# Optimization experiments

Hardware: AMD Instinct MI355X
Metric: run time of the kernel (lower is better)

Reference implementation:

```python
import jax, jax.numpy as jnp
import numpy as np

H = 128  # hidden_dim


def _lstm_dir(x, w_ih, w_hh, b, reverse):
    """Single-direction LSTM over x:[B,T,I]. PyTorch gate order (i,f,g,o)."""
    B = x.shape[0]
    gx = jnp.einsum('bti,gi->btg', x, w_ih) + b        # [B,T,4H] input-side gates, one batched GEMM
    gx = jnp.swapaxes(gx, 0, 1)                        # [T,B,4H]
    if reverse:
        gx = gx[::-1]

    def step(carry, g_x):
        h, c = carry
        g = g_x + h @ w_hh.T                           # [B,4H]
        i, f, gg, o = jnp.split(g, 4, axis=-1)
        i = jax.nn.sigmoid(i)
        f = jax.nn.sigmoid(f)
        gg = jnp.tanh(gg)
        o = jax.nn.sigmoid(o)
        c = f * c + i * gg
        h = o * jnp.tanh(c)
        return (h, c), h

    init = (jnp.zeros((B, H), x.dtype), jnp.zeros((B, H), x.dtype))
    (hT, cT), hs = jax.lax.scan(step, init, gx)        # hs:[T,B,H]
    hs = jnp.swapaxes(hs, 0, 1)                        # [B,T,H]
    if reverse:
        hs = hs[:, ::-1]
    return hs, hT, cT


def _bilstm_layer(x, pf, pb):
    hf, hTf, cTf = _lstm_dir(x, *pf, reverse=False)
    hb, hTb, cTb = _lstm_dir(x, *pb, reverse=True)
    return jnp.concatenate([hf, hb], axis=-1), (hTf, cTf), (hTb, cTb)


def setup_inputs() -> dict:
    key = jax.random.key(0)
    ks = jax.random.split(key, 13)
    s = 1.0 / np.sqrt(H)
    B, T, I = 256, 512, 24
    d = {"x": jax.random.normal(ks[0], (B, T, I), jnp.float32)}
    # layer 0 input dim = 24; layer 1 input dim = 2*H = 256
    dims = {"l0f": I, "l0b": I, "l1f": 2 * H, "l1b": 2 * H}
    i = 1
    for tag, din in dims.items():
        d[f"w_ih_{tag}"] = jax.random.uniform(ks[i], (4 * H, din), jnp.float32, -s, s); i += 1
        d[f"w_hh_{tag}"] = jax.random.uniform(ks[i], (4 * H, H), jnp.float32, -s, s); i += 1
        d[f"b_{tag}"] = jax.random.uniform(ks[i], (4 * H,), jnp.float32, -s, s); i += 1
    return d


def reference(x,
              w_ih_l0f, w_hh_l0f, b_l0f, w_ih_l0b, w_hh_l0b, b_l0b,
              w_ih_l1f, w_hh_l1f, b_l1f, w_ih_l1b, w_hh_l1b, b_l1b):
    # Layer 0 (bidirectional)
    y0, (hTf0, cTf0), (hTb0, cTb0) = _bilstm_layer(
        x, (w_ih_l0f, w_hh_l0f, b_l0f), (w_ih_l0b, w_hh_l0b, b_l0b))
    # Inter-layer dropout is identity in eval mode.
    # Layer 1 (bidirectional)
    y1, (hTf1, cTf1), (hTb1, cTb1) = _bilstm_layer(
        y0, (w_ih_l1f, w_hh_l1f, b_l1f), (w_ih_l1b, w_hh_l1b, b_l1b))
    # PyTorch h_n/c_n layout: [num_layers*num_dirs, B, H] ordered l0f,l0b,l1f,l1b
    h_n = jnp.stack([hTf0, hTb0, hTf1, hTb1], axis=0)
    c_n = jnp.stack([cTf0, cTb0, cTf1, cTb1], axis=0)
    return y1, h_n, c_n
```

## Files before the change

### kernel.cpp

```cpp
#include <hip/hip_runtime.h>
#include <hip/hip_bf16.h>
#include <stdint.h>

#define Bn 256
#define Tn 512
#define Hn 128
#define G4 512
#define Mn (Bn*Tn)

typedef __attribute__((ext_vector_type(8))) short s16x8;
typedef __attribute__((ext_vector_type(4))) float f32x4;

__device__ __forceinline__ float b2f(unsigned short u) {
    union { unsigned int i; float f; } v; v.i = ((unsigned int)u) << 16; return v.f;
}
__device__ __forceinline__ unsigned short f2b(float f) {
    union { float f; unsigned int i; } v; v.f = f;
    unsigned int x = v.i;
    unsigned int r = (x + 0x7FFFu + ((x >> 16) & 1u)) >> 16;
    return (unsigned short)r;
}
__device__ __forceinline__ unsigned int pk2(float a, float b) {
    __hip_bfloat162 t = __float22bfloat162_rn(make_float2(a, b));
    union { __hip_bfloat162 v; unsigned int u; } c; c.v = t; return c.u;
}
__device__ __forceinline__ s16x8 cvt8v(const float* p) {
    f32x4 a = *(const f32x4*)p;
    f32x4 b = *(const f32x4*)(p + 4);
    s16x8 r;
    r[0] = (short)f2b(a[0]); r[1] = (short)f2b(a[1]);
    r[2] = (short)f2b(a[2]); r[3] = (short)f2b(a[3]);
    r[4] = (short)f2b(b[0]); r[5] = (short)f2b(b[1]);
    r[6] = (short)f2b(b[2]); r[7] = (short)f2b(b[3]);
    return r;
}
__device__ __forceinline__ float sigm(float x) {
    return __builtin_amdgcn_rcpf(1.f + __expf(-x));
}
__device__ __forceinline__ float tanh_f(float x) {
    return 1.f - 2.f * __builtin_amdgcn_rcpf(1.f + __expf(2.f * x));
}
__device__ __forceinline__ void gload16(const void* gsrc, void* lds) {
    __builtin_amdgcn_global_load_lds(
        (const __attribute__((address_space(1))) unsigned int*)gsrc,
        (__attribute__((address_space(3))) unsigned int*)lds, 16, 0, 0);
}
__device__ __forceinline__ void ldsbar() {
    asm volatile("s_waitcnt lgkmcnt(0)\n\ts_barrier" ::: "memory");
}

__global__ __launch_bounds__(256)
void prep(const float* __restrict__ x,
          const float* __restrict__ w0f, const float* __restrict__ w0b,
          const float* __restrict__ w1f, const float* __restrict__ w1b,
          unsigned short* __restrict__ xb,
          unsigned short* __restrict__ w0bf,
          unsigned short* __restrict__ w1bf)
{
    int tid = blockIdx.x * 256 + threadIdx.x;
    int nthr = gridDim.x * 256;
    for (int idx = tid; idx < Mn * 32; idx += nthr) {
        int row = idx >> 5, col = idx & 31;
        xb[idx] = f2b(col < 24 ? x[row * 24 + col] : 0.f);
    }
    for (int idx = tid; idx < 2 * 512 * 32; idx += nthr) {
        int d = idx >> 14, rem = idx & 16383;
        int n = rem >> 5, col = rem & 31;
        const float* w = d ? w0b : w0f;
        w0bf[idx] = f2b(col < 24 ? w[n * 24 + col] : 0.f);
    }
    for (int idx = tid; idx < 2 * 512 * 256; idx += nthr) {
        int d = idx >> 17, rem = idx & 131071;
        const float* w = d ? w1b : w1f;
        w1bf[idx] = f2b(w[rem]);
    }
}

template<int BK, int KOUT>
__global__ __launch_bounds__(256, 2)
void gemm_tile(const unsigned short* __restrict__ A, int lda,
               const unsigned short* __restrict__ W,
               unsigned short* __restrict__ gx)
{
    constexpr int GR = BK / 8;
    constexpr int SWM = (GR >= 8) ? 7 : (GR - 1);
    constexpr int ASZ = 128 * BK * 2;
    constexpr int GOFF = (BK == 128) ? 0 : 2 * ASZ;
    constexpr int SMEM = 2 * ASZ + ((BK == 128) ? 0 : 4 * 16 * 68 * 4);
    __shared__ char smem[SMEM];
    unsigned short* Atile = (unsigned short*)smem;
    unsigned short* Btile = (unsigned short*)(smem + ASZ);

    const int K = BK * KOUT;
    const int mb = blockIdx.x;
    const int nb = blockIdx.y;
    const int dir = nb >> 2, ncol0 = (nb & 3) * 128;
    const int row0 = mb * 128;
    const unsigned short* Asrc = A + (size_t)row0 * lda;
    const unsigned short* Bsrc = W + (size_t)dir * 512 * K + (size_t)ncol0 * K;
    unsigned short* out = gx + (size_t)dir * Mn * G4;

    const int tid = threadIdx.x;
    const int w = tid >> 6, l = tid & 63;
    const int q = l >> 4, i = l & 15;
    const int wm = w >> 1, wn = w & 1;

    f32x4 acc[4][4];
#pragma unroll
    for (int a = 0; a < 4; ++a)
#pragma unroll
        for (int b = 0; b < 4; ++b) acc[a][b] = f32x4{0.f, 0.f, 0.f, 0.f};

    for (int ko = 0; ko < KOUT; ++ko) {
#pragma unroll
        for (int it = 0; it < (128 * GR) / 256; ++it) {
            int g = it * 256 + tid;
            int row = g / GR, p = g % GR;
            int gi = p ^ (row & SWM);
            gload16(Asrc + (size_t)row * lda + ko * BK + gi * 8,
                    (char*)Atile + g * 16);
        }
#pragma unroll
        for (int it = 0; it < (128 * GR) / 256; ++it) {
            int g = it * 256 + tid;
            int row = g / GR, p = g % GR;
            int gi = p ^ (row & SWM);
            gload16(Bsrc + (size_t)row * K + ko * BK + gi * 8,
                    (char*)Btile + g * 16);
        }
        __syncthreads();
#pragma unroll
        for (int kf = 0; kf < BK / 32; ++kf) {
            s16x8 af[4], bf[4];
#pragma unroll
            for (int mt = 0; mt < 4; ++mt) {
                int ar = wm * 64 + mt * 16 + i;
                int p = (kf * 4 + q) ^ (ar & SWM);
                af[mt] = *(const s16x8*)((char*)Atile + (ar * GR + p) * 16);
            }
#pragma unroll
            for (int nt = 0; nt < 4; ++nt) {
                int br = wn * 64 + nt * 16 + i;
                int p = (kf * 4 + q) ^ (br & SWM);
                bf[nt] = *(const s16x8*)((char*)Btile + (br * GR + p) * 16);
            }
#pragma unroll
            for (int mt = 0; mt < 4; ++mt)
#pragma unroll
                for (int nt = 0; nt < 4; ++nt)
                    acc[mt][nt] = __builtin_amdgcn_mfma_f32_16x16x32_bf16(
                        af[mt], bf[nt], acc[mt][nt], 0, 0, 0);
        }
        __syncthreads();
    }

    float* gbufw = (float*)(smem + GOFF) + w * (16 * 68);
#pragma unroll
    for (int mt = 0; mt < 4; ++mt) {
#pragma unroll
        for (int nt = 0; nt < 4; ++nt)
#pragma unroll
            for (int r = 0; r < 4; ++r)
                gbufw[(q * 4 + r) * 68 + nt * 16 + i] = acc[mt][nt][r];
        __syncthreads();
#pragma unroll
        for (int it2 = 0; it2 < 2; ++it2) {
            int rr = (l >> 3) + it2 * 8;
            int cc = (l & 7) * 8;
            const float* gsrc = gbufw + rr * 68 + cc;
            uint4 pv;
            pv.x = pk2(gsrc[0], gsrc[1]);
            pv.y = pk2(gsrc[2], gsrc[3]);
            pv.z = pk2(gsrc[4], gsrc[5]);
            pv.w = pk2(gsrc[6], gsrc[7]);
            *(uint4*)(out + (size_t)(row0 + wm * 64 + mt * 16 + rr) * G4
                          + ncol0 + wn * 64 + cc) = pv;
        }
        __syncthreads();
    }
}

template<int LAYER>
__global__ __launch_bounds__(256, 1)
void lstm_rec(const unsigned short* __restrict__ gx,
              const float* __restrict__ Whf,
              const float* __restrict__ Whb,
              const float* __restrict__ biasf,
              const float* __restrict__ biasb,
              float* __restrict__ y,
              unsigned short* __restrict__ y0b,
              float* __restrict__ hn,
              float* __restrict__ cn)
{
    const int b0  = blockIdx.x * 2;
    const int dir = blockIdx.y;
    const float* Wh   = dir ? Whb : Whf;
    const float* bias = dir ? biasb : biasf;
    const unsigned short* gxd = gx + (size_t)dir * Mn * G4;

    const int tid = threadIdx.x;
    const int w = tid >> 6;
    const int l = tid & 63;
    const int q = l >> 4, i = l & 15;
    const int u = q & 1;
    const int r = q >> 1;
    const int j = 32 * w + 16 * u + i;
    const int b = b0 + r;

    __shared__ __align__(16) unsigned short hbuf[2][160];

    for (int idx = tid; idx < 2 * 160; idx += 256)
        ((unsigned short*)hbuf)[idx] = 0;

    s16x8 wh[4][2][4];
#pragma unroll
    for (int g = 0; g < 4; ++g)
#pragma unroll
        for (int ut = 0; ut < 2; ++ut) {
            int n = 128 * g + 32 * w + 16 * ut + i;
#pragma unroll
            for (int kf = 0; kf < 4; ++kf)
                wh[g][ut][kf] = cvt8v(Wh + (size_t)n * Hn + kf * 32 + q * 8);
        }

    const float bi = bias[j],       bfv = bias[128 + j];
    const float bg = bias[256 + j], bo  = bias[384 + j];
    float c = 0.f, hlast = 0.f;

    const s16x8* ah0p = (const s16x8*)&hbuf[i >> 3][0 * 32 + q * 8];
    const s16x8* ah1p = (const s16x8*)&hbuf[i >> 3][1 * 32 + q * 8];
    const s16x8* ah2p = (const s16x8*)&hbuf[i >> 3][2 * 32 + q * 8];
    const s16x8* ah3p = (const s16x8*)&hbuf[i >> 3][3 * 32 + q * 8];
    unsigned short* hw = &hbuf[r][j];

    const intptr_t gstep = dir ? -(intptr_t)G4 : (intptr_t)G4;
    const unsigned short* p0 =
        gxd + ((size_t)b * Tn + (dir ? Tn - 1 : 0)) * G4 + j;
    const unsigned short* gp_pre = p0 + 8 * gstep;
    const intptr_t ystep = dir ? (intptr_t)-256 : (intptr_t)256;
    float* yp = y + ((size_t)b * Tn + (dir ? Tn - 1 : 0)) * 256 + dir * 128 + j;
    unsigned short* y0p =
        y0b + ((size_t)b * Tn + (dir ? Tn - 1 : 0)) * 256 + dir * 128 + j;

    unsigned short bufA[4][8], bufB[4][8];
#pragma unroll
    for (int f = 0; f < 8; ++f) {
        const unsigned short* gp = p0 + f * gstep;
        bufA[0][f] = gp[0];
        bufA[1][f] = gp[128];
        bufA[2][f] = gp[256];
        bufA[3][f] = gp[384];
    }

    __syncthreads();

    auto do8 = [&](unsigned short (&useB)[4][8], unsigned short (&ldB)[4][8],
                   int sb) {
#pragma unroll
        for (int f = 0; f < 8; ++f) {
            const int s = sb + f;

            s16x8 ah0 = *ah0p, ah1 = *ah1p, ah2 = *ah2p, ah3 = *ah3p;

            ldB[0][f] = gp_pre[0];
            ldB[1][f] = gp_pre[128];
            ldB[2][f] = gp_pre[256];
            ldB[3][f] = gp_pre[384];
            if (s < Tn - 9) gp_pre += gstep;
            const float pi = b2f(useB[0][f]) + bi;
            const float pf = b2f(useB[1][f]) + bfv;
            const float pg = b2f(useB[2][f]) + bg;
            const float po = b2f(useB[3][f]) + bo;

            f32x4 acc[4][2];
#pragma unroll
            for (int g = 0; g < 4; ++g)
#pragma unroll
                for (int ut = 0; ut < 2; ++ut)
                    acc[g][ut] = f32x4{0.f, 0.f, 0.f, 0.f};
#pragma unroll
            for (int g = 0; g < 4; ++g)
#pragma unroll
                for (int ut = 0; ut < 2; ++ut)
                    acc[g][ut] = __builtin_amdgcn_mfma_f32_16x16x32_bf16(
                        ah0, wh[g][ut][0], acc[g][ut], 0, 0, 0);
#pragma unroll
            for (int g = 0; g < 4; ++g)
#pragma unroll
                for (int ut = 0; ut < 2; ++ut)
                    acc[g][ut] = __builtin_amdgcn_mfma_f32_16x16x32_bf16(
                        ah1, wh[g][ut][1], acc[g][ut], 0, 0, 0);
#pragma unroll
            for (int g = 0; g < 4; ++g)
#pragma unroll
                for (int ut = 0; ut < 2; ++ut)
                    acc[g][ut] = __builtin_amdgcn_mfma_f32_16x16x32_bf16(
                        ah2, wh[g][ut][2], acc[g][ut], 0, 0, 0);
#pragma unroll
            for (int g = 0; g < 4; ++g)
#pragma unroll
                for (int ut = 0; ut < 2; ++ut)
                    acc[g][ut] = __builtin_amdgcn_mfma_f32_16x16x32_bf16(
                        ah3, wh[g][ut][3], acc[g][ut], 0, 0, 0);

            const float s_i = u ? acc[0][1][0] : acc[0][0][0];
            const float s_f = u ? acc[1][1][0] : acc[1][0][0];
            const float s_g = u ? acc[2][1][0] : acc[2][0][0];
            const float s_o = u ? acc[3][1][0] : acc[3][0][0];

            float g_i = s_i + pi;
            float g_f = s_f + pf;
            float g_g = s_g + pg;
            float g_o = s_o + po;
            float iv = sigm(g_i), fv = sigm(g_f), ov = sigm(g_o);
            float gv = tanh_f(g_g);
            c = fv * c + iv * gv;
            float h = ov * tanh_f(c);
            hlast = h;
            unsigned int hp;
            asm("v_cvt_pk_bf16_f32 %0, %1, %2" : "=v"(hp) : "v"(h), "v"(h));
            unsigned short hb = (unsigned short)hp;
            *hw = hb;
            if (LAYER == 0) *y0p = hb;
            else            *yp  = h;
            yp += ystep; y0p += ystep;

            ldsbar();
        }
    };

    for (int sb = 0; sb < Tn; sb += 16) {
        do8(bufA, bufB, sb);
        do8(bufB, bufA, sb + 8);
    }

    const int slot = LAYER * 2 + dir;
    hn[((size_t)slot * Bn + b) * Hn + j] = hlast;
    cn[((size_t)slot * Bn + b) * Hn + j] = c;
}

extern "C" void kernel_launch(void* const* d_in, const int* in_sizes, int n_in,
                              void* d_out, int out_size, void* d_ws, size_t ws_size,
                              hipStream_t stream)
{
    const float* x     = (const float*)d_in[0];
    const float* wih0f = (const float*)d_in[1];
    const float* whh0f = (const float*)d_in[2];
    const float* b0f   = (const float*)d_in[3];
    const float* wih0b = (const float*)d_in[4];
    const float* whh0b = (const float*)d_in[5];
    const float* b0b   = (const float*)d_in[6];
    const float* wih1f = (const float*)d_in[7];
    const float* whh1f = (const float*)d_in[8];
    const float* b1f   = (const float*)d_in[9];
    const float* wih1b = (const float*)d_in[10];
    const float* whh1b = (const float*)d_in[11];
    const float* b1b   = (const float*)d_in[12];

    float* y  = (float*)d_out;
    float* hn = y + (size_t)Mn * 256;
    float* cn = hn + (size_t)4 * Bn * Hn;
    unsigned short* gx = (unsigned short*)d_ws;

    unsigned short* scr  = (unsigned short*)d_out;
    unsigned short* y0b  = scr;
    unsigned short* xb   = scr + (size_t)Mn * 256;
    unsigned short* w0bf = xb  + (size_t)Mn * 32;
    unsigned short* w1bf = w0bf + 2 * 512 * 32;

    prep<<<2048, 256, 0, stream>>>(x, wih0f, wih0b, wih1f, wih1b, xb, w0bf, w1bf);

    dim3 gg(1024, 8), gb(256);
    dim3 rg(128, 2), rb(256);

    gemm_tile<32, 1><<<gg, gb, 0, stream>>>(xb, 32, w0bf, gx);
    lstm_rec<0><<<rg, rb, 0, stream>>>(gx, whh0f, whh0b, b0f, b0b, y, y0b, hn, cn);
    gemm_tile<128, 2><<<gg, gb, 0, stream>>>(y0b, 256, w1bf, gx);
    lstm_rec<1><<<rg, rb, 0, stream>>>(gx, whh1f, whh1b, b1f, b1b, y, y0b, hn, cn);
}
```

Measured before the change: 1.005 ms.

## Process two batch pairs per recurrent block to interleave independent MFMA chains

```diff
diff --git a/kernel.cpp b/kernel.cpp
--- a/kernel.cpp
+++ b/kernel.cpp
@@ -192,7 +192,7 @@
               float* __restrict__ hn,
               float* __restrict__ cn)
 {
-    const int b0  = blockIdx.x * 2;
+    const int pb  = blockIdx.x;
     const int dir = blockIdx.y;
     const float* Wh   = dir ? Whb : Whf;
     const float* bias = dir ? biasb : biasf;
@@ -205,11 +205,11 @@
     const int u = q & 1;
     const int r = q >> 1;
     const int j = 32 * w + 16 * u + i;
-    const int b = b0 + r;
-
-    __shared__ __align__(16) unsigned short hbuf[2][160];
-
-    for (int idx = tid; idx < 2 * 160; idx += 256)
+    const int b0 = pb * 4;
+
+    __shared__ __align__(16) unsigned short hbuf[4][160];
+
+    for (int idx = tid; idx < 4 * 160; idx += 256)
         ((unsigned short*)hbuf)[idx] = 0;
 
     s16x8 wh[4][2][4];
@@ -225,118 +225,141 @@
 
     const float bi = bias[j],       bfv = bias[128 + j];
     const float bg = bias[256 + j], bo  = bias[384 + j];
-    float c = 0.f, hlast = 0.f;
-
-    const s16x8* ah0p = (const s16x8*)&hbuf[i >> 3][0 * 32 + q * 8];
-    const s16x8* ah1p = (const s16x8*)&hbuf[i >> 3][1 * 32 + q * 8];
-    const s16x8* ah2p = (const s16x8*)&hbuf[i >> 3][2 * 32 + q * 8];
-    const s16x8* ah3p = (const s16x8*)&hbuf[i >> 3][3 * 32 + q * 8];
-    unsigned short* hw = &hbuf[r][j];
+    float cc[2] = {0.f, 0.f}, hl[2] = {0.f, 0.f};
+
+    const s16x8* ahp[2][4];
+    unsigned short* hw[2];
+#pragma unroll
+    for (int ch = 0; ch < 2; ++ch) {
+#pragma unroll
+        for (int kf = 0; kf < 4; ++kf)
+            ahp[ch][kf] = (const s16x8*)&hbuf[2 * ch + (i >> 3)][kf * 32 + q * 8];
+        hw[ch] = &hbuf[2 * ch + r][j];
+    }
 
     const intptr_t gstep = dir ? -(intptr_t)G4 : (intptr_t)G4;
-    const unsigned short* p0 =
-        gxd + ((size_t)b * Tn + (dir ? Tn - 1 : 0)) * G4 + j;
-    const unsigned short* gp_pre = p0 + 8 * gstep;
     const intptr_t ystep = dir ? (intptr_t)-256 : (intptr_t)256;
-    float* yp = y + ((size_t)b * Tn + (dir ? Tn - 1 : 0)) * 256 + dir * 128 + j;
-    unsigned short* y0p =
-        y0b + ((size_t)b * Tn + (dir ? Tn - 1 : 0)) * 256 + dir * 128 + j;
-
-    unsigned short bufA[4][8], bufB[4][8];
-#pragma unroll
-    for (int f = 0; f < 8; ++f) {
-        const unsigned short* gp = p0 + f * gstep;
-        bufA[0][f] = gp[0];
-        bufA[1][f] = gp[128];
-        bufA[2][f] = gp[256];
-        bufA[3][f] = gp[384];
-    }
+    const int t0 = dir ? Tn - 1 : 0;
+    const unsigned short* p0c[2];
+    const unsigned short* gp_pre[2];
+    float* ypp[2];
+    unsigned short* y0pp[2];
+#pragma unroll
+    for (int ch = 0; ch < 2; ++ch) {
+        const int b = b0 + 2 * ch + r;
+        p0c[ch]   = gxd + ((size_t)b * Tn + t0) * G4 + j;
+        gp_pre[ch] = p0c[ch] + 4 * gstep;
+        ypp[ch]   = y  + ((size_t)b * Tn + t0) * 256 + dir * 128 + j;
+        y0pp[ch]  = y0b + ((size_t)b * Tn + t0) * 256 + dir * 128 + j;
+    }
+
+    unsigned short bufA[2][4][4], bufB[2][4][4];
+#pragma unroll
+    for (int ch = 0; ch < 2; ++ch)
+#pragma unroll
+        for (int f = 0; f < 4; ++f) {
+            const unsigned short* gp = p0c[ch] + f * gstep;
+            bufA[ch][0][f] = gp[0];
+            bufA[ch][1][f] = gp[128];
+            bufA[ch][2][f] = gp[256];
+            bufA[ch][3][f] = gp[384];
+        }
 
     __syncthreads();
 
-    auto do8 = [&](unsigned short (&useB)[4][8], unsigned short (&ldB)[4][8],
-                   int sb) {
-#pragma unroll
-        for (int f = 0; f < 8; ++f) {
+    auto do4 = [&](unsigned short (&useB)[2][4][4],
+                   unsigned short (&ldB)[2][4][4], int sb) {
+#pragma unroll
+        for (int f = 0; f < 4; ++f) {
             const int s = sb + f;
 
-            s16x8 ah0 = *ah0p, ah1 = *ah1p, ah2 = *ah2p, ah3 = *ah3p;
-
-            ldB[0][f] = gp_pre[0];
-            ldB[1][f] = gp_pre[128];
-            ldB[2][f] = gp_pre[256];
-            ldB[3][f] = gp_pre[384];
-            if (s < Tn - 9) gp_pre += gstep;
-            const float pi = b2f(useB[0][f]) + bi;
-            const float pf = b2f(useB[1][f]) + bfv;
-            const float pg = b2f(useB[2][f]) + bg;
-            const float po = b2f(useB[3][f]) + bo;
-
-            f32x4 acc[4][2];
-#pragma unroll
-            for (int g = 0; g < 4; ++g)
-#pragma unroll
-                for (int ut = 0; ut < 2; ++ut)
-                    acc[g][ut] = f32x4{0.f, 0.f, 0.f, 0.f};
-#pragma unroll
-            for (int g = 0; g < 4; ++g)
-#pragma unroll
-                for (int ut = 0; ut < 2; ++ut)
-                    acc[g][ut] = __builtin_amdgcn_mfma_f32_16x16x32_bf16(
-                        ah0, wh[g][ut][0], acc[g][ut], 0, 0, 0);
-#pragma unroll
-            for (int g = 0; g < 4; ++g)
-#pragma unroll
-                for (int ut = 0; ut < 2; ++ut)
-                    acc[g][ut] = __builtin_amdgcn_mfma_f32_16x16x32_bf16(
-                        ah1, wh[g][ut][1], acc[g][ut], 0, 0, 0);
-#pragma unroll
-            for (int g = 0; g < 4; ++g)
-#pragma unroll
-                for (int ut = 0; ut < 2; ++ut)
-                    acc[g][ut] = __builtin_amdgcn_mfma_f32_16x16x32_bf16(
-                        ah2, wh[g][ut][2], acc[g][ut], 0, 0, 0);
-#pragma unroll
-            for (int g = 0; g < 4; ++g)
-#pragma unroll
-                for (int ut = 0; ut < 2; ++ut)
-                    acc[g][ut] = __builtin_amdgcn_mfma_f32_16x16x32_bf16(
-                        ah3, wh[g][ut][3], acc[g][ut], 0, 0, 0);
-
-            const float s_i = u ? acc[0][1][0] : acc[0][0][0];
-            const float s_f = u ? acc[1][1][0] : acc[1][0][0];
-            const float s_g = u ? acc[2][1][0] : acc[2][0][0];
-            const float s_o = u ? acc[3][1][0] : acc[3][0][0];
-
-            float g_i = s_i + pi;
-            float g_f = s_f + pf;
-            float g_g = s_g + pg;
-            float g_o = s_o + po;
-            float iv = sigm(g_i), fv = sigm(g_f), ov = sigm(g_o);
-            float gv = tanh_f(g_g);
-            c = fv * c + iv * gv;
-            float h = ov * tanh_f(c);
-            hlast = h;
-            unsigned int hp;
-            asm("v_cvt_pk_bf16_f32 %0, %1, %2" : "=v"(hp) : "v"(h), "v"(h));
-            unsigned short hb = (unsigned short)hp;
-            *hw = hb;
-            if (LAYER == 0) *y0p = hb;
-            else            *yp  = h;
-            yp += ystep; y0p += ystep;
+            s16x8 ah[2][4];
+#pragma unroll
+            for (int ch = 0; ch < 2; ++ch)
+#pragma unroll
+                for (int kf = 0; kf < 4; ++kf)
+                    ah[ch][kf] = *ahp[ch][kf];
+
+#pragma unroll
+            for (int ch = 0; ch < 2; ++ch) {
+                ldB[ch][0][f] = gp_pre[ch][0];
+                ldB[ch][1][f] = gp_pre[ch][128];
+                ldB[ch][2][f] = gp_pre[ch][256];
+                ldB[ch][3][f] = gp_pre[ch][384];
+            }
+            if (s < Tn - 5) { gp_pre[0] += gstep; gp_pre[1] += gstep; }
+
+            float pc[2][4];
+#pragma unroll
+            for (int ch = 0; ch < 2; ++ch) {
+                pc[ch][0] = b2f(useB[ch][0][f]) + bi;
+                pc[ch][1] = b2f(useB[ch][1][f]) + bfv;
+                pc[ch][2] = b2f(useB[ch][2][f]) + bg;
+                pc[ch][3] = b2f(useB[ch][3][f]) + bo;
+            }
+
+            f32x4 acc[2][4][2];
+#pragma unroll
+            for (int ch = 0; ch < 2; ++ch)
+#pragma unroll
+                for (int g = 0; g < 4; ++g)
+#pragma unroll
+                    for (int ut = 0; ut < 2; ++ut)
+                        acc[ch][g][ut] = f32x4{0.f, 0.f, 0.f, 0.f};
+#pragma unroll
+            for (int kf = 0; kf < 4; ++kf)
+#pragma unroll
+                for (int ch = 0; ch < 2; ++ch)
+#pragma unroll
+                    for (int g = 0; g < 4; ++g)
+#pragma unroll
+                        for (int ut = 0; ut < 2; ++ut)
+                            acc[ch][g][ut] =
+                                __builtin_amdgcn_mfma_f32_16x16x32_bf16(
+                                    ah[ch][kf], wh[g][ut][kf],
+                                    acc[ch][g][ut], 0, 0, 0);
+
+#pragma unroll
+            for (int ch = 0; ch < 2; ++ch) {
+                const float s_i = u ? acc[ch][0][1][0] : acc[ch][0][0][0];
+                const float s_f = u ? acc[ch][1][1][0] : acc[ch][1][0][0];
+                const float s_g = u ? acc[ch][2][1][0] : acc[ch][2][0][0];
+                const float s_o = u ? acc[ch][3][1][0] : acc[ch][3][0][0];
+
+                float g_i = s_i + pc[ch][0];
+                float g_f = s_f + pc[ch][1];
+                float g_g = s_g + pc[ch][2];
+                float g_o = s_o + pc[ch][3];
+                float iv = sigm(g_i), fv = sigm(g_f), ov = sigm(g_o);
+                float gv = tanh_f(g_g);
+                cc[ch] = fv * cc[ch] + iv * gv;
+                float h = ov * tanh_f(cc[ch]);
+                hl[ch] = h;
+                unsigned int hp;
+                asm("v_cvt_pk_bf16_f32 %0, %1, %2" : "=v"(hp) : "v"(h), "v"(h));
+                unsigned short hb = (unsigned short)hp;
+                *hw[ch] = hb;
+                if (LAYER == 0) *y0pp[ch] = hb;
+                else            *ypp[ch]  = h;
+                ypp[ch] += ystep; y0pp[ch] += ystep;
+            }
 
             ldsbar();
         }
     };
 
-    for (int sb = 0; sb < Tn; sb += 16) {
-        do8(bufA, bufB, sb);
-        do8(bufB, bufA, sb + 8);
+    for (int sb = 0; sb < Tn; sb += 8) {
+        do4(bufA, bufB, sb);
+        do4(bufB, bufA, sb + 4);
     }
 
     const int slot = LAYER * 2 + dir;
-    hn[((size_t)slot * Bn + b) * Hn + j] = hlast;
-    cn[((size_t)slot * Bn + b) * Hn + j] = c;
+#pragma unroll
+    for (int ch = 0; ch < 2; ++ch) {
+        const int b = b0 + 2 * ch + r;
+        hn[((size_t)slot * Bn + b) * Hn + j] = hl[ch];
+        cn[((size_t)slot * Bn + b) * Hn + j] = cc[ch];
+    }
 }
 
 extern "C" void kernel_launch(void* const* d_in, const int* in_sizes, int n_in,
@@ -371,7 +394,7 @@
     prep<<<2048, 256, 0, stream>>>(x, wih0f, wih0b, wih1f, wih1b, xb, w0bf, w1bf);
 
     dim3 gg(1024, 8), gb(256);
-    dim3 rg(128, 2), rb(256);
+    dim3 rg(64, 2), rb(256);
 
     gemm_tile<32, 1><<<gg, gb, 0, stream>>>(xb, 32, w0bf, gx);
     lstm_rec<0><<<rg, rb, 0, stream>>>(gx, whh0f, whh0b, b0f, b0b, y, y0b, hn, cn);
```

After: 1.188 ms. 1.18x slower.

## Assign one batch row per recurrent block and split MFMA accumulation chains

Applied to the files above, without the earlier changes.

```diff
diff --git a/kernel.cpp b/kernel.cpp
--- a/kernel.cpp
+++ b/kernel.cpp
@@ -181,7 +181,7 @@
 }
 
 template<int LAYER>
-__global__ __launch_bounds__(256, 1)
+__global__ __launch_bounds__(256, 2)
 void lstm_rec(const unsigned short* __restrict__ gx,
               const float* __restrict__ Whf,
               const float* __restrict__ Whb,
@@ -192,7 +192,7 @@
               float* __restrict__ hn,
               float* __restrict__ cn)
 {
-    const int b0  = blockIdx.x * 2;
+    const int b   = blockIdx.x;
     const int dir = blockIdx.y;
     const float* Wh   = dir ? Whb : Whf;
     const float* bias = dir ? biasb : biasf;
@@ -203,14 +203,12 @@
     const int l = tid & 63;
     const int q = l >> 4, i = l & 15;
     const int u = q & 1;
-    const int r = q >> 1;
     const int j = 32 * w + 16 * u + i;
-    const int b = b0 + r;
-
-    __shared__ __align__(16) unsigned short hbuf[2][160];
-
-    for (int idx = tid; idx < 2 * 160; idx += 256)
-        ((unsigned short*)hbuf)[idx] = 0;
+
+    __shared__ __align__(16) unsigned short hbuf[160];
+
+    for (int idx = tid; idx < 160; idx += 256)
+        hbuf[idx] = 0;
 
     s16x8 wh[4][2][4];
 #pragma unroll
@@ -227,24 +225,23 @@
     const float bg = bias[256 + j], bo  = bias[384 + j];
     float c = 0.f, hlast = 0.f;
 
-    const s16x8* ah0p = (const s16x8*)&hbuf[i >> 3][0 * 32 + q * 8];
-    const s16x8* ah1p = (const s16x8*)&hbuf[i >> 3][1 * 32 + q * 8];
-    const s16x8* ah2p = (const s16x8*)&hbuf[i >> 3][2 * 32 + q * 8];
-    const s16x8* ah3p = (const s16x8*)&hbuf[i >> 3][3 * 32 + q * 8];
-    unsigned short* hw = &hbuf[r][j];
+    const s16x8* ah0p = (const s16x8*)&hbuf[0 * 32 + q * 8];
+    const s16x8* ah1p = (const s16x8*)&hbuf[1 * 32 + q * 8];
+    const s16x8* ah2p = (const s16x8*)&hbuf[2 * 32 + q * 8];
+    const s16x8* ah3p = (const s16x8*)&hbuf[3 * 32 + q * 8];
+    unsigned short* hw = &hbuf[j];
 
     const intptr_t gstep = dir ? -(intptr_t)G4 : (intptr_t)G4;
-    const unsigned short* p0 =
-        gxd + ((size_t)b * Tn + (dir ? Tn - 1 : 0)) * G4 + j;
-    const unsigned short* gp_pre = p0 + 8 * gstep;
     const intptr_t ystep = dir ? (intptr_t)-256 : (intptr_t)256;
-    float* yp = y + ((size_t)b * Tn + (dir ? Tn - 1 : 0)) * 256 + dir * 128 + j;
-    unsigned short* y0p =
-        y0b + ((size_t)b * Tn + (dir ? Tn - 1 : 0)) * 256 + dir * 128 + j;
-
-    unsigned short bufA[4][8], bufB[4][8];
-#pragma unroll
-    for (int f = 0; f < 8; ++f) {
+    const int t0 = dir ? Tn - 1 : 0;
+    const unsigned short* p0 = gxd + ((size_t)b * Tn + t0) * G4 + j;
+    const unsigned short* gp_pre = p0 + 4 * gstep;
+    float* yp = y + ((size_t)b * Tn + t0) * 256 + dir * 128 + j;
+    unsigned short* y0p = y0b + ((size_t)b * Tn + t0) * 256 + dir * 128 + j;
+
+    unsigned short bufA[4][4], bufB[4][4];
+#pragma unroll
+    for (int f = 0; f < 4; ++f) {
         const unsigned short* gp = p0 + f * gstep;
         bufA[0][f] = gp[0];
         bufA[1][f] = gp[128];
@@ -254,10 +251,10 @@
 
     __syncthreads();
 
-    auto do8 = [&](unsigned short (&useB)[4][8], unsigned short (&ldB)[4][8],
+    auto do4 = [&](unsigned short (&useB)[4][4], unsigned short (&ldB)[4][4],
                    int sb) {
 #pragma unroll
-        for (int f = 0; f < 8; ++f) {
+        for (int f = 0; f < 4; ++f) {
             const int s = sb + f;
 
             s16x8 ah0 = *ah0p, ah1 = *ah1p, ah2 = *ah2p, ah3 = *ah3p;
@@ -266,47 +263,54 @@
             ldB[1][f] = gp_pre[128];
             ldB[2][f] = gp_pre[256];
             ldB[3][f] = gp_pre[384];
-            if (s < Tn - 9) gp_pre += gstep;
+            if (s < Tn - 5) gp_pre += gstep;
+
             const float pi = b2f(useB[0][f]) + bi;
             const float pf = b2f(useB[1][f]) + bfv;
             const float pg = b2f(useB[2][f]) + bg;
             const float po = b2f(useB[3][f]) + bo;
 
-            f32x4 acc[4][2];
+            f32x4 a0[4][2], a1[4][2];
+#pragma unroll
+            for (int g = 0; g < 4; ++g)
+#pragma unroll
+                for (int ut = 0; ut < 2; ++ut) {
+                    a0[g][ut] = f32x4{0.f, 0.f, 0.f, 0.f};
+                    a1[g][ut] = f32x4{0.f, 0.f, 0.f, 0.f};
+                }
 #pragma unroll
             for (int g = 0; g < 4; ++g)
 #pragma unroll
                 for (int ut = 0; ut < 2; ++ut)
-                    acc[g][ut] = f32x4{0.f, 0.f, 0.f, 0.f};
+                    a0[g][ut] = __builtin_amdgcn_mfma_f32_16x16x32_bf16(
+                        ah0, wh[g][ut][0], a0[g][ut], 0, 0, 0);
 #pragma unroll
             for (int g = 0; g < 4; ++g)
 #pragma unroll
                 for (int ut = 0; ut < 2; ++ut)
-                    acc[g][ut] = __builtin_amdgcn_mfma_f32_16x16x32_bf16(
-                        ah0, wh[g][ut][0], acc[g][ut], 0, 0, 0);
+                    a1[g][ut] = __builtin_amdgcn_mfma_f32_16x16x32_bf16(
+                        ah1, wh[g][ut][1], a1[g][ut], 0, 0, 0);
 #pragma unroll
             for (int g = 0; g < 4; ++g)
 #pragma unroll
                 for (int ut = 0; ut < 2; ++ut)
-                    acc[g][ut] = __builtin_amdgcn_mfma_f32_16x16x32_bf16(
-                        ah1, wh[g][ut][1], acc[g][ut], 0, 0, 0);
+                    a0[g][ut] = __builtin_amdgcn_mfma_f32_16x16x32_bf16(
+                        ah2, wh[g][ut][2], a0[g][ut], 0, 0, 0);
 #pragma unroll
             for (int g = 0; g < 4; ++g)
 #pragma unroll
                 for (int ut = 0; ut < 2; ++ut)
-                    acc[g][ut] = __builtin_amdgcn_mfma_f32_16x16x32_bf16(
-                        ah2, wh[g][ut][2], acc[g][ut], 0, 0, 0);
-#pragma unroll
-            for (int g = 0; g < 4; ++g)
-#pragma unroll
-                for (int ut = 0; ut < 2; ++ut)
-                    acc[g][ut] = __builtin_amdgcn_mfma_f32_16x16x32_bf16(
-                        ah3, wh[g][ut][3], acc[g][ut], 0, 0, 0);
-
-            const float s_i = u ? acc[0][1][0] : acc[0][0][0];
-            const float s_f = u ? acc[1][1][0] : acc[1][0][0];
-            const float s_g = u ? acc[2][1][0] : acc[2][0][0];
-            const float s_o = u ? acc[3][1][0] : acc[3][0][0];
+                    a1[g][ut] = __builtin_amdgcn_mfma_f32_16x16x32_bf16(
+                        ah3, wh[g][ut][3], a1[g][ut], 0, 0, 0);
+
+            const float s_i = (u ? a0[0][1][0] : a0[0][0][0])
+                            + (u ? a1[0][1][0] : a1[0][0][0]);
+            const float s_f = (u ? a0[1][1][0] : a0[1][0][0])
+                            + (u ? a1[1][1][0] : a1[1][0][0]);
+            const float s_g = (u ? a0[2][1][0] : a0[2][0][0])
+                            + (u ? a1[2][1][0] : a1[2][0][0]);
+            const float s_o = (u ? a0[3][1][0] : a0[3][0][0])
+                            + (u ? a1[3][1][0] : a1[3][0][0]);
 
             float g_i = s_i + pi;
             float g_f = s_f + pf;
@@ -329,9 +333,9 @@
         }
     };
 
-    for (int sb = 0; sb < Tn; sb += 16) {
-        do8(bufA, bufB, sb);
-        do8(bufB, bufA, sb + 8);
+    for (int sb = 0; sb < Tn; sb += 8) {
+        do4(bufA, bufB, sb);
+        do4(bufB, bufA, sb + 4);
     }
 
     const int slot = LAYER * 2 + dir;
@@ -371,7 +375,7 @@
     prep<<<2048, 256, 0, stream>>>(x, wih0f, wih0b, wih1f, wih1b, xb, w0bf, w1bf);
 
     dim3 gg(1024, 8), gb(256);
-    dim3 rg(128, 2), rb(256);
+    dim3 rg(256, 2), rb(256);
 
     gemm_tile<32, 1><<<gg, gb, 0, stream>>>(xb, 32, w0bf, gx);
     lstm_rec<0><<<rg, rb, 0, stream>>>(gx, whh0f, whh0b, b0f, b0b, y, y0b, hn, cn);
```

After: 1.174 ms. 16.8% more time.

## Store gate preactivations time-blocked for vector loads and double-buffer hidden state

Applied to the files above, without the earlier changes.

```diff
diff --git a/kernel.cpp b/kernel.cpp
--- a/kernel.cpp
+++ b/kernel.cpp
@@ -9,6 +9,7 @@
 #define Mn (Bn*Tn)
 
 typedef __attribute__((ext_vector_type(8))) short s16x8;
+typedef __attribute__((ext_vector_type(8))) unsigned short u16x8;
 typedef __attribute__((ext_vector_type(4))) float f32x4;
 
 __device__ __forceinline__ float b2f(unsigned short u) {
@@ -19,10 +20,6 @@
     unsigned int x = v.i;
     unsigned int r = (x + 0x7FFFu + ((x >> 16) & 1u)) >> 16;
     return (unsigned short)r;
-}
-__device__ __forceinline__ unsigned int pk2(float a, float b) {
-    __hip_bfloat162 t = __float22bfloat162_rn(make_float2(a, b));
-    union { __hip_bfloat162 v; unsigned int u; } c; c.v = t; return c.u;
 }
 __device__ __forceinline__ s16x8 cvt8v(const float* p) {
     f32x4 a = *(const f32x4*)p;
@@ -168,13 +165,16 @@
             int rr = (l >> 3) + it2 * 8;
             int cc = (l & 7) * 8;
             const float* gsrc = gbufw + rr * 68 + cc;
-            uint4 pv;
-            pv.x = pk2(gsrc[0], gsrc[1]);
-            pv.y = pk2(gsrc[2], gsrc[3]);
-            pv.z = pk2(gsrc[4], gsrc[5]);
-            pv.w = pk2(gsrc[6], gsrc[7]);
-            *(uint4*)(out + (size_t)(row0 + wm * 64 + mt * 16 + rr) * G4
-                          + ncol0 + wn * 64 + cc) = pv;
+            const int mrow = row0 + wm * 64 + mt * 16 + rr;
+            const int bb = mrow >> 9, t = mrow & 511;
+            const int te = dir ? (Tn - 1 - t) : t;
+            const int tb = te >> 3, tin = te & 7;
+            const int n0 = ncol0 + wn * 64 + cc;
+            unsigned short* ob =
+                out + ((((size_t)bb * 64 + tb) * 512 + n0) << 3) + tin;
+#pragma unroll
+            for (int k2 = 0; k2 < 8; ++k2)
+                ob[(size_t)k2 * 8] = f2b(gsrc[k2]);
         }
         __syncthreads();
     }
@@ -207,9 +207,9 @@
     const int j = 32 * w + 16 * u + i;
     const int b = b0 + r;
 
-    __shared__ __align__(16) unsigned short hbuf[2][160];
-
-    for (int idx = tid; idx < 2 * 160; idx += 256)
+    __shared__ __align__(16) unsigned short hbuf[2][2][160];
+
+    for (int idx = tid; idx < 2 * 2 * 160; idx += 256)
         ((unsigned short*)hbuf)[idx] = 0;
 
     s16x8 wh[4][2][4];
@@ -227,50 +227,52 @@
     const float bg = bias[256 + j], bo  = bias[384 + j];
     float c = 0.f, hlast = 0.f;
 
-    const s16x8* ah0p = (const s16x8*)&hbuf[i >> 3][0 * 32 + q * 8];
-    const s16x8* ah1p = (const s16x8*)&hbuf[i >> 3][1 * 32 + q * 8];
-    const s16x8* ah2p = (const s16x8*)&hbuf[i >> 3][2 * 32 + q * 8];
-    const s16x8* ah3p = (const s16x8*)&hbuf[i >> 3][3 * 32 + q * 8];
-    unsigned short* hw = &hbuf[r][j];
-
-    const intptr_t gstep = dir ? -(intptr_t)G4 : (intptr_t)G4;
-    const unsigned short* p0 =
-        gxd + ((size_t)b * Tn + (dir ? Tn - 1 : 0)) * G4 + j;
-    const unsigned short* gp_pre = p0 + 8 * gstep;
+    const s16x8* ahp[2][4];
+    unsigned short* hwp[2];
+#pragma unroll
+    for (int par = 0; par < 2; ++par) {
+#pragma unroll
+        for (int kf = 0; kf < 4; ++kf)
+            ahp[par][kf] =
+                (const s16x8*)&hbuf[par][i >> 3][kf * 32 + q * 8];
+        hwp[par] = &hbuf[par][r][j];
+    }
+
+    const unsigned short* gbase =
+        gxd + (size_t)b * (64 * 512 * 8) + ((size_t)j << 3);
+
     const intptr_t ystep = dir ? (intptr_t)-256 : (intptr_t)256;
-    float* yp = y + ((size_t)b * Tn + (dir ? Tn - 1 : 0)) * 256 + dir * 128 + j;
-    unsigned short* y0p =
-        y0b + ((size_t)b * Tn + (dir ? Tn - 1 : 0)) * 256 + dir * 128 + j;
-
-    unsigned short bufA[4][8], bufB[4][8];
-#pragma unroll
-    for (int f = 0; f < 8; ++f) {
-        const unsigned short* gp = p0 + f * gstep;
-        bufA[0][f] = gp[0];
-        bufA[1][f] = gp[128];
-        bufA[2][f] = gp[256];
-        bufA[3][f] = gp[384];
-    }
+    const int t0 = dir ? Tn - 1 : 0;
+    float* yp = y + ((size_t)b * Tn + t0) * 256 + dir * 128 + j;
+    unsigned short* y0p = y0b + ((size_t)b * Tn + t0) * 256 + dir * 128 + j;
+
+    u16x8 cur[4], nxt[4];
+#pragma unroll
+    for (int g = 0; g < 4; ++g)
+        cur[g] = *(const u16x8*)(gbase + (size_t)g * 1024);
 
     __syncthreads();
 
-    auto do8 = [&](unsigned short (&useB)[4][8], unsigned short (&ldB)[4][8],
-                   int sb) {
+    for (int tb = 0; tb < 64; ++tb) {
+        const int tbn = (tb < 63) ? tb + 1 : 63;
 #pragma unroll
         for (int f = 0; f < 8; ++f) {
-            const int s = sb + f;
-
-            s16x8 ah0 = *ah0p, ah1 = *ah1p, ah2 = *ah2p, ah3 = *ah3p;
-
-            ldB[0][f] = gp_pre[0];
-            ldB[1][f] = gp_pre[128];
-            ldB[2][f] = gp_pre[256];
-            ldB[3][f] = gp_pre[384];
-            if (s < Tn - 9) gp_pre += gstep;
-            const float pi = b2f(useB[0][f]) + bi;
-            const float pf = b2f(useB[1][f]) + bfv;
-            const float pg = b2f(useB[2][f]) + bg;
-            const float po = b2f(useB[3][f]) + bo;
+            const int par = f & 1;
+
+            s16x8 ah0 = *ahp[par][0], ah1 = *ahp[par][1];
+            s16x8 ah2 = *ahp[par][2], ah3 = *ahp[par][3];
+
+            if (f == 2) {
+#pragma unroll
+                for (int g = 0; g < 4; ++g)
+                    nxt[g] = *(const u16x8*)(gbase + (size_t)tbn * 4096
+                                                   + (size_t)g * 1024);
+            }
+
+            const float pi = b2f(cur[0][f]) + bi;
+            const float pf = b2f(cur[1][f]) + bfv;
+            const float pg = b2f(cur[2][f]) + bg;
+            const float po = b2f(cur[3][f]) + bo;
 
             f32x4 acc[4][2];
 #pragma unroll
@@ -320,18 +322,15 @@
             unsigned int hp;
             asm("v_cvt_pk_bf16_f32 %0, %1, %2" : "=v"(hp) : "v"(h), "v"(h));
             unsigned short hb = (unsigned short)hp;
-            *hw = hb;
+            *hwp[par ^ 1] = hb;
             if (LAYER == 0) *y0p = hb;
             else            *yp  = h;
             yp += ystep; y0p += ystep;
 
             ldsbar();
         }
-    };
-
-    for (int sb = 0; sb < Tn; sb += 16) {
-        do8(bufA, bufB, sb);
-        do8(bufB, bufA, sb + 8);
+#pragma unroll
+        for (int g = 0; g < 4; ++g) cur[g] = nxt[g];
     }
 
     const int slot = LAYER * 2 + dir;
```

New measurement: 985.1 us. 1.02x faster.
